# Performance work log

Hardware: AMD Instinct MI355X
Metric: run time of the kernel (lower is better)

Reference implementation:

```python
import jax, jax.numpy as jnp
import numpy as np


def setup_inputs() -> dict:
    key = jax.random.key(0)
    k1, k2 = jax.random.split(key)
    B, C, H, W = 16, 2, 512, 512
    probs = jax.random.uniform(k1, (B, C, H, W), dtype=jnp.float32)
    gt = jax.random.randint(k2, (B, 1, H, W), 0, 2, dtype=jnp.int32)
    return {"probs": probs, "gt": gt}


def _edt_sq(mask):
    """Exact squared Euclidean distance transform of the background.

    mask: [H, W] bool, True = foreground (gt == 1).
    Returns [H, W] float32: squared distance from each pixel to nearest
    foreground pixel (0 at foreground), matching
    scipy.ndimage.distance_transform_edt(1 - gt)**2.
    Separable algorithm: exact 1D pass along rows (nearest fg row per
    column via cummax/cummin), then min-plus with squared column offsets.
    """
    H, W = mask.shape
    rows = jnp.arange(H, dtype=jnp.float32)[:, None]  # [H, 1]
    BIG = float(2 * (H + W))  # sentinel: farther than any real distance
    # nearest foreground row at-or-above / at-or-below each pixel, per column
    f = jax.lax.cummax(jnp.where(mask, rows, -BIG), axis=0)            # [H, W]
    b = jax.lax.cummin(jnp.where(mask, rows, BIG + H), axis=0, reverse=True)
    d1 = jnp.minimum((rows - f) ** 2, (b - rows) ** 2)  # column-wise sq dist [H, W]
    cols = jnp.arange(W, dtype=jnp.float32)
    jdiff = (cols[:, None] - cols[None, :]) ** 2        # [W_out, W_in]
    # exact 2D: d2[i, j] = min_{j'} (d1[i, j'] + (j - j')^2)
    return jnp.min(d1[:, None, :] + jdiff[None, :, :], axis=-1)  # [H, W]


def reference(probs, gt):
    mask = gt[:, 0].astype(bool)                 # [B, H, W]
    # sequential over batch (lax.map) to bound the [H, W, W] intermediate
    dist = jnp.sqrt(jax.lax.map(_edt_sq, mask))  # [B, H, W]
    return jnp.mean(probs[:, 0] * dist)
```

## Files before the change

### kernel.cpp

```cpp
#include <hip/hip_runtime.h>
#include <math.h>

constexpr int BATCH = 16;
constexpr int H = 512;
constexpr int W = 512;
constexpr int NBLOCKS = BATCH * H;
constexpr int R = 8;
constexpr float INV_N = 1.0f / (float)(16 * 512 * 512);

__global__ __launch_bounds__(512) void boundary_loss_main(
    const float* __restrict__ probs,
    const int* __restrict__ gt,
    float* __restrict__ partial)
{
    const int row = blockIdx.x;
    const int b = row >> 9;
    const int i = row & 511;
    const int j = threadIdx.x;

    const int* colp = gt + (size_t)b * (H * W) + j;
    const int up_max = i;
    const int dn_max = H - 1 - i;

    const float p = probs[(size_t)b * 2 * H * W + (size_t)i * W + j];

    int w[2 * R + 1];
    #pragma unroll
    for (int k = 0; k < 2 * R + 1; ++k) {
        int r = i - R + k;
        r = max(0, min(H - 1, r));
        w[k] = colp[r * W];
    }

    int tu = -1, td = -1;
    if (w[R]) { tu = 0; td = 0; }
    #pragma unroll
    for (int t = 1; t <= R; ++t) {
        if (tu < 0 && t <= up_max && w[R - t]) tu = t;
        if (td < 0 && t <= dn_max && w[R + t]) td = t;
    }

    if (tu < 0 && up_max > R) {
        int t = R + 1;
        while (tu < 0 && t <= up_max) {
            int v[4];
            #pragma unroll
            for (int k = 0; k < 4; ++k) {
                int ti = min(t + k, up_max);
                v[k] = colp[(i - ti) * W];
            }
            #pragma unroll
            for (int k = 0; k < 4; ++k)
                if (tu < 0 && t + k <= up_max && v[k]) tu = t + k;
            t += 4;
        }
    }
    if (td < 0 && dn_max > R) {
        int t = R + 1;
        while (td < 0 && t <= dn_max) {
            int v[4];
            #pragma unroll
            for (int k = 0; k < 4; ++k) {
                int ti = min(t + k, dn_max);
                v[k] = colp[(i + ti) * W];
            }
            #pragma unroll
            for (int k = 0; k < 4; ++k)
                if (td < 0 && t + k <= dn_max && v[k]) td = t + k;
            t += 4;
        }
    }

    const int du = (tu >= 0) ? tu * tu : (i + 2048) * (i + 2048);
    const int dd = (td >= 0) ? td * td : (2560 - i) * (2560 - i);
    const int d1 = min(du, dd);

    __shared__ int d1row[W];
    d1row[j] = d1;
    __syncthreads();

    int best = d1;
    #pragma unroll
    for (int t = 1; t <= 4; ++t) {
        const int tt = t * t;
        const int cl = d1row[max(j - t, 0)] + tt;
        const int cr = d1row[min(j + t, W - 1)] + tt;
        if (j - t >= 0) best = min(best, cl);
        if (j + t < W)  best = min(best, cr);
    }
    if (best > 25) {
        int t = 5;
        while (t < W && t * t < best) {
            #pragma unroll
            for (int k = 0; k < 2; ++k) {
                const int tk = t + k;
                const int tt = tk * tk;
                const int cl = d1row[max(j - tk, 0)] + tt;
                const int cr = d1row[min(j + tk, W - 1)] + tt;
                if (j - tk >= 0) best = min(best, cl);
                if (j + tk < W)  best = min(best, cr);
            }
            t += 2;
        }
    }

    float v = p * sqrtf((float)best);

    for (int off = 32; off > 0; off >>= 1)
        v += __shfl_down(v, off, 64);
    __shared__ float wsum[8];
    const int lane = j & 63;
    const int wid = j >> 6;
    if (lane == 0) wsum[wid] = v;
    __syncthreads();
    if (j == 0) {
        float s = 0.0f;
        #pragma unroll
        for (int wi = 0; wi < 8; ++wi) s += wsum[wi];
        partial[row] = s;
    }
}

__global__ __launch_bounds__(512) void boundary_loss_reduce(
    const float* __restrict__ partial,
    float* __restrict__ out)
{
    const int j = threadIdx.x;
    float s = 0.0f;
    #pragma unroll
    for (int k = 0; k < NBLOCKS / 512; ++k)
        s += partial[k * 512 + j];
    for (int off = 32; off > 0; off >>= 1)
        s += __shfl_down(s, off, 64);
    __shared__ float wsum[8];
    const int lane = j & 63;
    const int wid = j >> 6;
    if (lane == 0) wsum[wid] = s;
    __syncthreads();
    if (j == 0) {
        float tot = 0.0f;
        #pragma unroll
        for (int wi = 0; wi < 8; ++wi) tot += wsum[wi];
        out[0] = tot * INV_N;
    }
}

extern "C" void kernel_launch(void* const* d_in, const int* in_sizes, int n_in,
                              void* d_out, int out_size, void* d_ws, size_t ws_size,
                              hipStream_t stream) {
    const float* probs = (const float*)d_in[0];
    const int* gt = (const int*)d_in[1];
    float* out = (float*)d_out;
    float* partial = (float*)d_ws;

    boundary_loss_main<<<dim3(NBLOCKS), dim3(W), 0, stream>>>(probs, gt, partial);
    boundary_loss_reduce<<<dim3(1), dim3(512), 0, stream>>>(partial, out);
}
```

Baseline: 107.0 us.

## Process four rows per block to share the vertical gt window loads

Each block now handles four consecutive image rows instead of one. It loads a single vertical window of ROWS+2R gt values per column and reuses it for the short-range search of all four rows, which cuts redundant global loads and block launch overhead. The four per-row d1 results go into a larger shared array for the horizontal min-plus pass. In exchange, the grid has a quarter as many blocks and each thread does sequential per-row work with more registers, which can reduce parallelism and occupancy.

```diff
diff --git a/kernel.cpp b/kernel.cpp
--- a/kernel.cpp
+++ b/kernel.cpp
@@ -4,8 +4,9 @@
 constexpr int BATCH = 16;
 constexpr int H = 512;
 constexpr int W = 512;
-constexpr int NBLOCKS = BATCH * H;
 constexpr int R = 8;
+constexpr int ROWS = 4;
+constexpr int GRID = BATCH * H / ROWS;
 constexpr float INV_N = 1.0f / (float)(16 * 512 * 512);
 
 __global__ __launch_bounds__(512) void boundary_loss_main(
@@ -13,98 +14,105 @@
     const int* __restrict__ gt,
     float* __restrict__ partial)
 {
-    const int row = blockIdx.x;
-    const int b = row >> 9;
-    const int i = row & 511;
+    const int blk = blockIdx.x;
+    const int b = blk >> 7;
+    const int i0 = (blk & 127) * ROWS;
     const int j = threadIdx.x;
 
     const int* colp = gt + (size_t)b * (H * W) + j;
-    const int up_max = i;
-    const int dn_max = H - 1 - i;
 
-    const float p = probs[(size_t)b * 2 * H * W + (size_t)i * W + j];
+    const float* prow = probs + (size_t)b * 2 * H * W + (size_t)i0 * W + j;
+    float p[ROWS];
+    #pragma unroll
+    for (int r = 0; r < ROWS; ++r) p[r] = prow[r * W];
 
-    int w[2 * R + 1];
+    int w[ROWS + 2 * R];
     #pragma unroll
-    for (int k = 0; k < 2 * R + 1; ++k) {
-        int r = i - R + k;
-        r = max(0, min(H - 1, r));
-        w[k] = colp[r * W];
+    for (int k = 0; k < ROWS + 2 * R; ++k) {
+        int rr = i0 - R + k;
+        rr = max(0, min(H - 1, rr));
+        w[k] = colp[rr * W];
     }
 
-    int tu = -1, td = -1;
-    if (w[R]) { tu = 0; td = 0; }
+    int d1v[ROWS];
     #pragma unroll
-    for (int t = 1; t <= R; ++t) {
-        if (tu < 0 && t <= up_max && w[R - t]) tu = t;
-        if (td < 0 && t <= dn_max && w[R + t]) td = t;
+    for (int r = 0; r < ROWS; ++r) {
+        const int ir = i0 + r;
+        const int up_max = ir;
+        const int dn_max = H - 1 - ir;
+        int tu = -1, td = -1;
+        if (w[R + r]) { tu = 0; td = 0; }
+        #pragma unroll
+        for (int t = 1; t <= R; ++t) {
+            if (tu < 0 && t <= up_max && w[R + r - t]) tu = t;
+            if (td < 0 && t <= dn_max && w[R + r + t]) td = t;
+        }
+        if (tu < 0 && up_max > R) {
+            int t = R + 1;
+            while (tu < 0 && t <= up_max) {
+                int v[4];
+                #pragma unroll
+                for (int k = 0; k < 4; ++k)
+                    v[k] = colp[(ir - min(t + k, up_max)) * W];
+                #pragma unroll
+                for (int k = 0; k < 4; ++k)
+                    if (tu < 0 && t + k <= up_max && v[k]) tu = t + k;
+                t += 4;
+            }
+        }
+        if (td < 0 && dn_max > R) {
+            int t = R + 1;
+            while (td < 0 && t <= dn_max) {
+                int v[4];
+                #pragma unroll
+                for (int k = 0; k < 4; ++k)
+                    v[k] = colp[(ir + min(t + k, dn_max)) * W];
+                #pragma unroll
+                for (int k = 0; k < 4; ++k)
+                    if (td < 0 && t + k <= dn_max && v[k]) td = t + k;
+                t += 4;
+            }
+        }
+        const int du = (tu >= 0) ? tu * tu : (ir + 2048) * (ir + 2048);
+        const int dd = (td >= 0) ? td * td : (2560 - ir) * (2560 - ir);
+        d1v[r] = min(du, dd);
     }
 
-    if (tu < 0 && up_max > R) {
-        int t = R + 1;
-        while (tu < 0 && t <= up_max) {
-            int v[4];
-            #pragma unroll
-            for (int k = 0; k < 4; ++k) {
-                int ti = min(t + k, up_max);
-                v[k] = colp[(i - ti) * W];
-            }
-            #pragma unroll
-            for (int k = 0; k < 4; ++k)
-                if (tu < 0 && t + k <= up_max && v[k]) tu = t + k;
-            t += 4;
-        }
-    }
-    if (td < 0 && dn_max > R) {
-        int t = R + 1;
-        while (td < 0 && t <= dn_max) {
-            int v[4];
-            #pragma unroll
-            for (int k = 0; k < 4; ++k) {
-                int ti = min(t + k, dn_max);
-                v[k] = colp[(i + ti) * W];
-            }
-            #pragma unroll
-            for (int k = 0; k < 4; ++k)
-                if (td < 0 && t + k <= dn_max && v[k]) td = t + k;
-            t += 4;
-        }
-    }
-
-    const int du = (tu >= 0) ? tu * tu : (i + 2048) * (i + 2048);
-    const int dd = (td >= 0) ? td * td : (2560 - i) * (2560 - i);
-    const int d1 = min(du, dd);
-
-    __shared__ int d1row[W];
-    d1row[j] = d1;
+    __shared__ int d1s[ROWS][W];
+    #pragma unroll
+    for (int r = 0; r < ROWS; ++r) d1s[r][j] = d1v[r];
     __syncthreads();
 
-    int best = d1;
+    float v = 0.0f;
     #pragma unroll
-    for (int t = 1; t <= 4; ++t) {
-        const int tt = t * t;
-        const int cl = d1row[max(j - t, 0)] + tt;
-        const int cr = d1row[min(j + t, W - 1)] + tt;
-        if (j - t >= 0) best = min(best, cl);
-        if (j + t < W)  best = min(best, cr);
+    for (int r = 0; r < ROWS; ++r) {
+        int best = d1v[r];
+        const int* drow = d1s[r];
+        #pragma unroll
+        for (int t = 1; t <= 4; ++t) {
+            const int tt = t * t;
+            const int cl = drow[max(j - t, 0)] + tt;
+            const int cr = drow[min(j + t, W - 1)] + tt;
+            if (j - t >= 0) best = min(best, cl);
+            if (j + t < W)  best = min(best, cr);
+        }
+        if (best > 25) {
+            int t = 5;
+            while (t < W && t * t < best) {
+                #pragma unroll
+                for (int k = 0; k < 2; ++k) {
+                    const int tk = t + k;
+                    const int tt = tk * tk;
+                    const int cl = drow[max(j - tk, 0)] + tt;
+                    const int cr = drow[min(j + tk, W - 1)] + tt;
+                    if (j - tk >= 0) best = min(best, cl);
+                    if (j + tk < W)  best = min(best, cr);
+                }
+                t += 2;
+            }
+        }
+        v += p[r] * sqrtf((float)best);
     }
-    if (best > 25) {
-        int t = 5;
-        while (t < W && t * t < best) {
-            #pragma unroll
-            for (int k = 0; k < 2; ++k) {
-                const int tk = t + k;
-                const int tt = tk * tk;
-                const int cl = d1row[max(j - tk, 0)] + tt;
-                const int cr = d1row[min(j + tk, W - 1)] + tt;
-                if (j - tk >= 0) best = min(best, cl);
-                if (j + tk < W)  best = min(best, cr);
-            }
-            t += 2;
-        }
-    }
-
-    float v = p * sqrtf((float)best);
 
     for (int off = 32; off > 0; off >>= 1)
         v += __shfl_down(v, off, 64);
@@ -117,7 +125,7 @@
         float s = 0.0f;
         #pragma unroll
         for (int wi = 0; wi < 8; ++wi) s += wsum[wi];
-        partial[row] = s;
+        partial[blk] = s;
     }
 }
 
@@ -128,7 +136,7 @@
     const int j = threadIdx.x;
     float s = 0.0f;
     #pragma unroll
-    for (int k = 0; k < NBLOCKS / 512; ++k)
+    for (int k = 0; k < GRID / 512; ++k)
         s += partial[k * 512 + j];
     for (int off = 32; off > 0; off >>= 1)
         s += __shfl_down(s, off, 64);
@@ -153,6 +161,6 @@
     float* out = (float*)d_out;
     float* partial = (float*)d_ws;
 
-    boundary_loss_main<<<dim3(NBLOCKS), dim3(W), 0, stream>>>(probs, gt, partial);
+    boundary_loss_main<<<dim3(GRID), dim3(W), 0, stream>>>(probs, gt, partial);
     boundary_loss_reduce<<<dim3(1), dim3(512), 0, stream>>>(partial, out);
 }
```

Result: faster. 99.49 us (-7.0%).
